# Optimization experiments

Measured on AMD Instinct MI355X. Metric: run time of the kernel, lower is better.

The kernel has to match this reference:

```python
import jax, jax.numpy as jnp
import numpy as np

B, S, D, H = 2, 2048, 1024, 16
DH = D // H  # 64


def setup_inputs() -> dict:
    key = jax.random.key(0)
    ks = jax.random.split(key, 6)
    scale = 1.0 / np.sqrt(D)
    x = jax.random.normal(ks[0], (B, S, D), dtype=jnp.float32)
    Wq = jax.random.normal(ks[1], (D, D), dtype=jnp.float32) * scale
    Wk = jax.random.normal(ks[2], (D, D), dtype=jnp.float32) * scale
    Wv = jax.random.normal(ks[3], (D, D), dtype=jnp.float32) * scale
    Wo = jax.random.normal(ks[4], (D, D), dtype=jnp.float32) * scale
    zeros = jnp.zeros((D,), dtype=jnp.float32)
    return {"x": x, "Wq": Wq, "bq": zeros, "Wk": Wk, "bk": zeros,
            "Wv": Wv, "bv": zeros, "Wo": Wo, "bo": zeros}


def reference(x, Wq, bq, Wk, bk, Wv, bv, Wo, bo):
    # x: [B, S, D]
    def split_heads(t):
        # [B, S, D] -> [B, H, S, DH]
        return t.reshape(B, S, H, DH).transpose(0, 2, 1, 3)

    q = split_heads(x @ Wq + bq)
    k = split_heads(x @ Wk + bk)
    v = split_heads(x @ Wv + bv)

    scores = jnp.einsum('bhqd,bhkd->bhqk', q, k) / jnp.sqrt(jnp.float32(DH))
    weights = jax.nn.softmax(scores, axis=-1)          # [B, H, S, S]
    o = jnp.einsum('bhqk,bhkd->bhqd', weights, v)       # [B, H, S, DH]
    o = o.transpose(0, 2, 1, 3).reshape(B, S, D)        # merge heads
    return o @ Wo + bo
```

## Files before the change

kernel.cpp:

```cpp
#include <hip/hip_runtime.h>
#include <hip/hip_bf16.h>

#define DEV __device__ __forceinline__

typedef short bf16x8 __attribute__((ext_vector_type(8)));
typedef float f32x4 __attribute__((ext_vector_type(4)));
typedef unsigned int u32;
typedef unsigned int u32x4 __attribute__((ext_vector_type(4)));

constexpr int BB = 2, SS = 2048, DD = 1024, HH = 16, DHD = 64;
constexpr int MM = BB * SS;
#define QSC 0.1803368801111f

#if __has_builtin(__builtin_amdgcn_exp2f)
#define EXP2(x) __builtin_amdgcn_exp2f(x)
#else
#define EXP2(x) exp2f(x)
#endif

DEV unsigned short f2bf(float f) {
    union { float f; unsigned int u; } v; v.f = f;
    return (unsigned short)((v.u + 0x8000u) >> 16);
}
#if __has_builtin(__builtin_amdgcn_perm)
DEV u32 pk2bf(float a, float b) {
    union { float f; u32 u; } ua, ub; ua.f = a; ub.f = b;
    return __builtin_amdgcn_perm(ub.u + 0x8000u, ua.u + 0x8000u, 0x07060302u);
}
#else
DEV u32 pk2bf(float a, float b) {
    union { float f; u32 u; } ua, ub; ua.f = a; ub.f = b;
    return ((ua.u + 0x8000u) >> 16) | ((ub.u + 0x8000u) & 0xffff0000u);
}
#endif

DEV u32 cvtpk2bf(float a, float b) {
    u32 r;
    asm("v_cvt_pk_bf16_f32 %0, %1, %2" : "=v"(r) : "v"(a), "v"(b));
    return r;
}

DEV bf16x8 ld_bf16x8(const unsigned short* p) { return *(const bf16x8*)p; }

DEV void gl16(const unsigned short* g, unsigned short* l) {
    __builtin_amdgcn_global_load_lds(
        (const __attribute__((address_space(1))) u32*)g,
        (__attribute__((address_space(3))) u32*)l, 16, 0, 0);
}

__global__ void prep(const float* __restrict__ x, unsigned short* __restrict__ xb,
                     const float* __restrict__ W0, const float* __restrict__ W1,
                     const float* __restrict__ W2, const float* __restrict__ W3,
                     unsigned short* __restrict__ WtBase) {
    __shared__ float tile[32][33];
    int blk = blockIdx.x;
    if (blk < 4096) {
        int i = blk * 256 + threadIdx.x;
        float4 v = ((const float4*)x)[i];
        uint2 o;
        o.x = pk2bf(v.x, v.y);
        o.y = pk2bf(v.z, v.w);
        ((uint2*)xb)[i] = o;
        return;
    }
    blk -= 4096;
    int wsel = blk >> 10;
    const float* W = (wsel == 0) ? W0 : (wsel == 1) ? W1 : (wsel == 2) ? W2 : W3;
    unsigned short* Wt = WtBase + (size_t)wsel * DD * DD;
    int t = blk & 1023;
    int n0 = (t & 31) * 32, k0 = (t >> 5) * 32;
    int tx = threadIdx.x & 31, ty = threadIdx.x >> 5;
    #pragma unroll
    for (int i = 0; i < 4; ++i)
        tile[ty + 8 * i][tx] = W[(size_t)(k0 + ty + 8 * i) * DD + n0 + tx];
    __syncthreads();
    #pragma unroll
    for (int i = 0; i < 4; ++i)
        Wt[(size_t)(n0 + ty + 8 * i) * DD + k0 + tx] = f2bf(tile[tx][ty + 8 * i]);
}

__global__ __launch_bounds__(256) void qkv_gemm(
    const unsigned short* __restrict__ xb,
    const unsigned short* __restrict__ WtBase,
    const float* __restrict__ bq, const float* __restrict__ bk, const float* __restrict__ bv,
    unsigned short* __restrict__ Qb, unsigned short* __restrict__ Kb, unsigned short* __restrict__ Vt)
{
    __shared__ __align__(16) unsigned short Ald[2][128 * 32];
    __shared__ __align__(16) unsigned short Bld[2][128 * 32];

    const int z = blockIdx.z;
    const unsigned short* Wt = WtBase + (size_t)z * DD * DD;
    const float* bias = (z == 0) ? bq : (z == 1) ? bk : bv;

    const int gid2 = blockIdx.x + 8 * blockIdx.y;
    const int xk = gid2 & 7, o = gid2 >> 3;
    const int xe = (xk & 1) * 4 + (o & 3);
    const int ye = (xk >> 1) * 8 + (o >> 2);
    const int m0g = ye * 128;
    const int n0g = xe * 128;

    const int wave = threadIdx.x >> 6, lane = threadIdx.x & 63;
    const int quad = lane >> 4, lcol = lane & 15;
    const int mb = (wave & 1) * 64, nb = (wave >> 1) * 64;

    f32x4 acc[4][4];
    #pragma unroll
    for (int i = 0; i < 4; ++i)
        #pragma unroll
        for (int j = 0; j < 4; ++j) acc[i][j] = (f32x4){0.f, 0.f, 0.f, 0.f};

    auto stage = [&](int ks, int bf) {
        #pragma unroll
        for (int i = 0; i < 4; ++i) {
            int j = wave * 4 + i;
            if (j < 8) {
                int bi = j * 64 + lane;
                int row = bi >> 2, p = (bi & 3) ^ ((row >> 1) & 3);
                gl16(xb + (size_t)(m0g + row) * DD + ks + p * 8, &Ald[bf][j * 512]);
            } else {
                int jj = j - 8;
                int bi = jj * 64 + lane;
                int row = bi >> 2, p = (bi & 3) ^ ((row >> 1) & 3);
                gl16(Wt + (size_t)(n0g + row) * DD + ks + p * 8, &Bld[bf][jj * 512]);
            }
        }
    };

    stage(0, 0);
    __syncthreads();

    for (int kk = 0; kk < 32; ++kk) {
        int bf = kk & 1;
        if (kk + 1 < 32) stage((kk + 1) * 32, (kk + 1) & 1);
        bf16x8 af[4], bfr[4];
        #pragma unroll
        for (int mt = 0; mt < 4; ++mt) {
            int row = mb + mt * 16 + lcol;
            af[mt] = ld_bf16x8(&Ald[bf][(row * 4 + (quad ^ ((row >> 1) & 3))) * 8]);
        }
        #pragma unroll
        for (int nt = 0; nt < 4; ++nt) {
            int row = nb + nt * 16 + lcol;
            bfr[nt] = ld_bf16x8(&Bld[bf][(row * 4 + (quad ^ ((row >> 1) & 3))) * 8]);
        }
        if (z < 2) {
            #pragma unroll
            for (int mt = 0; mt < 4; ++mt)
                #pragma unroll
                for (int nt = 0; nt < 4; ++nt)
                    acc[mt][nt] = __builtin_amdgcn_mfma_f32_16x16x32_bf16(bfr[nt], af[mt], acc[mt][nt], 0, 0, 0);
        } else {
            #pragma unroll
            for (int mt = 0; mt < 4; ++mt)
                #pragma unroll
                for (int nt = 0; nt < 4; ++nt)
                    acc[mt][nt] = __builtin_amdgcn_mfma_f32_16x16x32_bf16(af[mt], bfr[nt], acc[mt][nt], 0, 0, 0);
        }
        __syncthreads();
    }

    if (z < 2) {
        unsigned short* dst = (z == 0) ? Qb : Kb;
        const float sc = (z == 0) ? QSC : 1.0f;
        #pragma unroll
        for (int mt = 0; mt < 4; ++mt)
            #pragma unroll
            for (int nt = 0; nt < 4; ++nt) {
                int m = m0g + mb + mt * 16 + lcol;
                int nbt = n0g + nb + nt * 16 + quad * 4;
                int b = m >> 11, s = m & (SS - 1);
                int h = nbt >> 6, dh0 = nbt & 63;
                float4 bv4 = *(const float4*)&bias[nbt];
                uint2 o2;
                o2.x = pk2bf((acc[mt][nt][0] + bv4.x) * sc, (acc[mt][nt][1] + bv4.y) * sc);
                o2.y = pk2bf((acc[mt][nt][2] + bv4.z) * sc, (acc[mt][nt][3] + bv4.w) * sc);
                *(uint2*)&dst[(((size_t)b * HH + h) * SS + s) * DHD + dh0] = o2;
            }
    } else {
        #pragma unroll
        for (int mt = 0; mt < 4; ++mt)
            #pragma unroll
            for (int nt = 0; nt < 4; ++nt) {
                int n = n0g + nb + nt * 16 + lcol;
                int mbt = m0g + mb + mt * 16 + quad * 4;
                int h = n >> 6, dh = n & 63;
                int b = mbt >> 11, s0 = mbt & (SS - 1);
                float bvv = bias[n];
                uint2 o2;
                o2.x = pk2bf(acc[mt][nt][0] + bvv, acc[mt][nt][1] + bvv);
                o2.y = pk2bf(acc[mt][nt][2] + bvv, acc[mt][nt][3] + bvv);
                *(uint2*)&Vt[(((size_t)b * HH + h) * DHD + dh) * SS + s0] = o2;
            }
    }
}

__global__ __launch_bounds__(512, 4) void attn(
    const unsigned short* __restrict__ Qb,
    const unsigned short* __restrict__ Kb,
    const unsigned short* __restrict__ Vt,
    unsigned short* __restrict__ Ob)
{
    __shared__ __align__(16) unsigned short Kld[2][64 * 64];
    __shared__ __align__(16) unsigned short Vld[2][64 * 64];

    const int g = blockIdx.y * gridDim.x + blockIdx.x;
    const int bh = (g & 7) * 4 + ((g >> 3) & 3);
    const int qt = g >> 5;
    const int b = bh >> 4, h = bh & (HH - 1);
    const unsigned short* Qbh = Qb + (size_t)bh * SS * DHD;
    const unsigned short* Kbh = Kb + (size_t)bh * SS * DHD;
    const unsigned short* Vbh = Vt + (size_t)bh * DHD * SS;

    const int wave = threadIdx.x >> 6, lane = threadIdx.x & 63;
    const int quad = lane >> 4, lcol = lane & 15;
    const int rowbase = qt * 128 + wave * 16;

    bf16x8 qf0 = ld_bf16x8(Qbh + (size_t)(rowbase + lcol) * DHD + quad * 8);
    bf16x8 qf1 = ld_bf16x8(Qbh + (size_t)(rowbase + lcol) * DHD + 32 + quad * 8);

    auto krow = [&](int kf2, int j) {
        return kf2 * 32 + ((lcol >> 2) << 3) + j * 4 + (lcol & 3);
    };
    auto kswz = [](int r) { return (r & 3) | (((r >> 3) & 1) << 2); };

    auto stage = [&](int c, int bf) {
        int kb = c * 64;
        #pragma unroll
        for (int i = 0; i < 2; ++i) {
            int j = wave * 2 + i;
            if (j < 8) {
                int bi = j * 64 + lane;
                int r = bi >> 3, p = (bi & 7) ^ ((r & 3) | (((r >> 3) & 1) << 2));
                gl16(Kbh + (size_t)(kb + r) * DHD + p * 8, &Kld[bf][j * 512]);
            } else {
                int jj = j - 8;
                int bi = jj * 64 + lane;
                int dh = bi >> 3, p = (bi & 7) ^ (dh & 7);
                gl16(Vbh + (size_t)dh * SS + kb + p * 8, &Vld[bf][jj * 512]);
            }
        }
    };

    stage(0, 0);
    __syncthreads();

    float m0 = -1e30f;
    #pragma unroll
    for (int kf2 = 0; kf2 < 2; ++kf2)
        #pragma unroll
        for (int j = 0; j < 2; ++j) {
            int kr = krow(kf2, j), sw = kswz(kr);
            bf16x8 ka0 = ld_bf16x8(&Kld[0][(kr * 8 + (quad ^ sw)) * 8]);
            bf16x8 ka1 = ld_bf16x8(&Kld[0][(kr * 8 + ((quad + 4) ^ sw)) * 8]);
            f32x4 s = (f32x4){0.f, 0.f, 0.f, 0.f};
            s = __builtin_amdgcn_mfma_f32_16x16x32_bf16(ka0, qf0, s, 0, 0, 0);
            s = __builtin_amdgcn_mfma_f32_16x16x32_bf16(ka1, qf1, s, 0, 0, 0);
            #pragma unroll
            for (int r = 0; r < 4; ++r) m0 = fmaxf(m0, s[r]);
        }
    #pragma unroll
    for (int msk = 1; msk < 64; msk <<= 1) m0 = fmaxf(m0, __shfl_xor(m0, msk, 64));
    const f32x4 minit = (f32x4){-m0, -m0, -m0, -m0};

    f32x4 oacc[4];
    #pragma unroll
    for (int nt = 0; nt < 4; ++nt) oacc[nt] = (f32x4){0.f, 0.f, 0.f, 0.f};
    float ps = 0.f;

    for (int c = 0; c < 32; ++c) {
        int bf = c & 1;
        if (c + 1 < 32) stage(c + 1, (c + 1) & 1);

        bf16x8 paf[2];
        #pragma unroll
        for (int kf2 = 0; kf2 < 2; ++kf2) {
            u32 w[4];
            #pragma unroll
            for (int j = 0; j < 2; ++j) {
                int kr = krow(kf2, j), sw = kswz(kr);
                bf16x8 ka0 = ld_bf16x8(&Kld[bf][(kr * 8 + (quad ^ sw)) * 8]);
                bf16x8 ka1 = ld_bf16x8(&Kld[bf][(kr * 8 + ((quad + 4) ^ sw)) * 8]);
                f32x4 s = minit;
                s = __builtin_amdgcn_mfma_f32_16x16x32_bf16(ka0, qf0, s, 0, 0, 0);
                s = __builtin_amdgcn_mfma_f32_16x16x32_bf16(ka1, qf1, s, 0, 0, 0);
                float e0 = EXP2(s[0]), e1 = EXP2(s[1]);
                float e2 = EXP2(s[2]), e3 = EXP2(s[3]);
                ps += (e0 + e1) + (e2 + e3);
                w[j * 2]     = cvtpk2bf(e0, e1);
                w[j * 2 + 1] = cvtpk2bf(e2, e3);
            }
            union { u32x4 u; bf16x8 v; } pu;
            pu.u = (u32x4){w[0], w[1], w[2], w[3]};
            paf[kf2] = pu.v;
        }

        #pragma unroll
        for (int kf2 = 0; kf2 < 2; ++kf2) {
            #pragma unroll
            for (int nt = 0; nt < 4; ++nt) {
                int dh = nt * 16 + lcol;
                bf16x8 vb = ld_bf16x8(&Vld[bf][(dh * 8 + ((kf2 * 4 + quad) ^ (dh & 7))) * 8]);
                oacc[nt] = __builtin_amdgcn_mfma_f32_16x16x32_bf16(paf[kf2], vb, oacc[nt], 0, 0, 0);
            }
        }
        __syncthreads();
    }

    ps += __shfl_xor(ps, 16, 64);
    ps += __shfl_xor(ps, 32, 64);
    float inv = 1.0f / ps;
    #pragma unroll
    for (int r = 0; r < 4; ++r) {
        float iv = __shfl(inv, quad * 4 + r, 64);
        int srow = rowbase + quad * 4 + r;
        size_t base = (((size_t)b * SS + srow) * HH + h) * DHD;
        #pragma unroll
        for (int nt = 0; nt < 4; ++nt)
            Ob[base + nt * 16 + lcol] = f2bf(oacc[nt][r] * iv);
    }
}

__global__ __launch_bounds__(256) void out_gemm(
    const unsigned short* __restrict__ Ob,
    const unsigned short* __restrict__ Wto,
    const float* __restrict__ bo,
    float* __restrict__ out)
{
    __shared__ __align__(16) unsigned short Wld[2][128 * 64];
    __shared__ __align__(16) unsigned short Old[2][64 * 64];

    const int m0g = blockIdx.y * 64;
    const int n0g = blockIdx.x * 128;
    const int wave = threadIdx.x >> 6, lane = threadIdx.x & 63;
    const int quad = lane >> 4, lcol = lane & 15;
    const int nb = wave * 32;

    f32x4 acc[2][4];
    #pragma unroll
    for (int i = 0; i < 2; ++i)
        #pragma unroll
        for (int j = 0; j < 4; ++j) acc[i][j] = (f32x4){0.f, 0.f, 0.f, 0.f};

    auto stage = [&](int ks, int bf) {
        #pragma unroll
        for (int i = 0; i < 6; ++i) {
            int j = wave * 6 + i;
            if (j < 16) {
                int bi = j * 64 + lane;
                int r = bi >> 3, p = (bi & 7) ^ (r & 7);
                gl16(Wto + (size_t)(n0g + r) * DD + ks + p * 8, &Wld[bf][j * 512]);
            } else {
                int jj = j - 16;
                int bi = jj * 64 + lane;
                int r = bi >> 3, p = (bi & 7) ^ (r & 7);
                gl16(Ob + (size_t)(m0g + r) * DD + ks + p * 8, &Old[bf][jj * 512]);
            }
        }
    };

    stage(0, 0);
    __syncthreads();

    for (int kk = 0; kk < 16; ++kk) {
        int bf = kk & 1;
        if (kk + 1 < 16) stage((kk + 1) * 64, (kk + 1) & 1);
        #pragma unroll
        for (int kh = 0; kh < 2; ++kh) {
            bf16x8 wf[2], of[4];
            #pragma unroll
            for (int i = 0; i < 2; ++i) {
                int row = nb + i * 16 + lcol;
                wf[i] = ld_bf16x8(&Wld[bf][(row * 8 + ((kh * 4 + quad) ^ (row & 7))) * 8]);
            }
            #pragma unroll
            for (int j = 0; j < 4; ++j) {
                int row = j * 16 + lcol;
                of[j] = ld_bf16x8(&Old[bf][(row * 8 + ((kh * 4 + quad) ^ (row & 7))) * 8]);
            }
            #pragma unroll
            for (int i = 0; i < 2; ++i)
                #pragma unroll
                for (int j = 0; j < 4; ++j)
                    acc[i][j] = __builtin_amdgcn_mfma_f32_16x16x32_bf16(wf[i], of[j], acc[i][j], 0, 0, 0);
        }
        __syncthreads();
    }

    #pragma unroll
    for (int i = 0; i < 2; ++i) {
        int n4 = n0g + nb + i * 16 + quad * 4;
        float4 bv4 = *(const float4*)&bo[n4];
        #pragma unroll
        for (int j = 0; j < 4; ++j) {
            int token = m0g + j * 16 + lcol;
            float4 o;
            o.x = acc[i][j][0] + bv4.x;
            o.y = acc[i][j][1] + bv4.y;
            o.z = acc[i][j][2] + bv4.z;
            o.w = acc[i][j][3] + bv4.w;
            *(float4*)&out[(size_t)token * DD + n4] = o;
        }
    }
}

extern "C" void kernel_launch(void* const* d_in, const int* in_sizes, int n_in,
                              void* d_out, int out_size, void* d_ws, size_t ws_size,
                              hipStream_t stream)
{
    const float* x  = (const float*)d_in[0];
    const float* Wq = (const float*)d_in[1];
    const float* bq = (const float*)d_in[2];
    const float* Wk = (const float*)d_in[3];
    const float* bk = (const float*)d_in[4];
    const float* Wv = (const float*)d_in[5];
    const float* bv = (const float*)d_in[6];
    const float* Wo = (const float*)d_in[7];
    const float* bo = (const float*)d_in[8];
    float* out = (float*)d_out;

    unsigned short* ws = (unsigned short*)d_ws;
    unsigned short* Wt  = ws;
    unsigned short* Wto = Wt + 3 * (size_t)DD * DD;
    unsigned short* Qb  = Wt + 4 * (size_t)DD * DD;
    unsigned short* Kb  = Qb + (size_t)MM * DD;
    unsigned short* Vt  = Kb + (size_t)MM * DD;
    unsigned short* xb  = Vt + (size_t)MM * DD;
    unsigned short* Ob  = xb;

    prep<<<8192, 256, 0, stream>>>(x, xb, Wq, Wk, Wv, Wo, Wt);

    qkv_gemm<<<dim3(8, 32, 3), 256, 0, stream>>>(xb, Wt, bq, bk, bv, Qb, Kb, Vt);

    attn<<<dim3(16, 32), 512, 0, stream>>>(Qb, Kb, Vt, Ob);

    out_gemm<<<dim3(DD / 128, MM / 64), 256, 0, stream>>>(Ob, Wto, bo, out);
}
```

Measured before the change: 196.8 us.

## Restructure QKV GEMM into 256x256 tiles with deeper async pipeline

The QKV projection GEMM moves from 128x128 tiles with 256 threads to 256x256 tiles with 512 threads (8 waves, 128x64 per wave) on a 1D grid of 192 blocks with an XCD-aware remap. The K loop now stages 64-wide K tiles in two 32-wide halves across double buffers, with explicit vmcnt waits, barriers, sched_barriers and s_setprio around MFMA clusters so global loads overlap compute. The aim is more data reuse per LDS load and better latency hiding. The cost is more registers and LDS per block, and only 192 blocks, which may underfill the 256 CUs.

Result: slower. 229.6 us (+16.7%).

```diff
diff --git a/kernel.cpp b/kernel.cpp
--- a/kernel.cpp
+++ b/kernel.cpp
@@ -79,118 +79,163 @@
         Wt[(size_t)(n0 + ty + 8 * i) * DD + k0 + tx] = f2bf(tile[tx][ty + 8 * i]);
 }
 
-__global__ __launch_bounds__(256) void qkv_gemm(
+__global__ __launch_bounds__(512, 2) void qkv_gemm(
     const unsigned short* __restrict__ xb,
     const unsigned short* __restrict__ WtBase,
     const float* __restrict__ bq, const float* __restrict__ bk, const float* __restrict__ bv,
     unsigned short* __restrict__ Qb, unsigned short* __restrict__ Kb, unsigned short* __restrict__ Vt)
 {
-    __shared__ __align__(16) unsigned short Ald[2][128 * 32];
-    __shared__ __align__(16) unsigned short Bld[2][128 * 32];
-
-    const int z = blockIdx.z;
+    __shared__ __align__(16) unsigned short AL[2][2][256 * 32];
+    __shared__ __align__(16) unsigned short BL[2][2][256 * 32];
+
+    const int d = blockIdx.x;
+    const int w = (d & 7) * 24 + (d >> 3);
+    const int xe = w & 3, ye = (w >> 2) & 15, z = w >> 6;
+    const int m0g = ye * 256, n0g = xe * 256;
+
     const unsigned short* Wt = WtBase + (size_t)z * DD * DD;
     const float* bias = (z == 0) ? bq : (z == 1) ? bk : bv;
-
-    const int gid2 = blockIdx.x + 8 * blockIdx.y;
-    const int xk = gid2 & 7, o = gid2 >> 3;
-    const int xe = (xk & 1) * 4 + (o & 3);
-    const int ye = (xk >> 1) * 8 + (o >> 2);
-    const int m0g = ye * 128;
-    const int n0g = xe * 128;
+    const bool zlt2 = (z < 2);
 
     const int wave = threadIdx.x >> 6, lane = threadIdx.x & 63;
     const int quad = lane >> 4, lcol = lane & 15;
-    const int mb = (wave & 1) * 64, nb = (wave >> 1) * 64;
-
-    f32x4 acc[4][4];
-    #pragma unroll
-    for (int i = 0; i < 4; ++i)
+    const int wr = wave >> 2, wc = wave & 3;
+
+    f32x4 acc[8][4];
+    #pragma unroll
+    for (int i = 0; i < 8; ++i)
         #pragma unroll
         for (int j = 0; j < 4; ++j) acc[i][j] = (f32x4){0.f, 0.f, 0.f, 0.f};
 
-    auto stage = [&](int ks, int bf) {
-        #pragma unroll
-        for (int i = 0; i < 4; ++i) {
-            int j = wave * 4 + i;
-            if (j < 8) {
-                int bi = j * 64 + lane;
-                int row = bi >> 2, p = (bi & 3) ^ ((row >> 1) & 3);
-                gl16(xb + (size_t)(m0g + row) * DD + ks + p * 8, &Ald[bf][j * 512]);
-            } else {
-                int jj = j - 8;
-                int bi = jj * 64 + lane;
-                int row = bi >> 2, p = (bi & 3) ^ ((row >> 1) & 3);
-                gl16(Wt + (size_t)(n0g + row) * DD + ks + p * 8, &Bld[bf][jj * 512]);
-            }
-        }
-    };
-
-    stage(0, 0);
-    __syncthreads();
-
-    for (int kk = 0; kk < 32; ++kk) {
-        int bf = kk & 1;
-        if (kk + 1 < 32) stage((kk + 1) * 32, (kk + 1) & 1);
-        bf16x8 af[4], bfr[4];
-        #pragma unroll
-        for (int mt = 0; mt < 4; ++mt) {
-            int row = mb + mt * 16 + lcol;
-            af[mt] = ld_bf16x8(&Ald[bf][(row * 4 + (quad ^ ((row >> 1) & 3))) * 8]);
-        }
-        #pragma unroll
-        for (int nt = 0; nt < 4; ++nt) {
-            int row = nb + nt * 16 + lcol;
-            bfr[nt] = ld_bf16x8(&Bld[bf][(row * 4 + (quad ^ ((row >> 1) & 3))) * 8]);
-        }
-        if (z < 2) {
-            #pragma unroll
-            for (int mt = 0; mt < 4; ++mt)
+    auto stageA = [&](int t, int ks, int bf) {
+        #pragma unroll
+        for (int i = 0; i < 2; ++i) {
+            int j = wave * 2 + i;
+            int bi = j * 64 + lane;
+            int row = bi >> 2, p = (bi & 3) ^ ((row >> 1) & 3);
+            gl16(xb + (size_t)(m0g + row) * DD + t * 64 + ks * 32 + p * 8, &AL[bf][ks][j * 512]);
+        }
+    };
+    auto stageB = [&](int t, int ks, int bf) {
+        #pragma unroll
+        for (int i = 0; i < 2; ++i) {
+            int j = wave * 2 + i;
+            int bi = j * 64 + lane;
+            int row = bi >> 2, p = (bi & 3) ^ ((row >> 1) & 3);
+            gl16(Wt + (size_t)(n0g + row) * DD + t * 64 + ks * 32 + p * 8, &BL[bf][ks][j * 512]);
+        }
+    };
+
+    auto lda = [&](int bf, int ks, int mt) {
+        int r = wr * 128 + mt * 16 + lcol;
+        return ld_bf16x8(&AL[bf][ks][(r * 4 + (quad ^ ((r >> 1) & 3))) * 8]);
+    };
+    auto ldb = [&](int bf, int ks, int nt) {
+        int r = wc * 64 + nt * 16 + lcol;
+        return ld_bf16x8(&BL[bf][ks][(r * 4 + (quad ^ ((r >> 1) & 3))) * 8]);
+    };
+
+    auto mm16 = [&](bf16x8* a4, bf16x8* b4, int mtb) {
+        if (zlt2) {
+            #pragma unroll
+            for (int i = 0; i < 4; ++i)
                 #pragma unroll
                 for (int nt = 0; nt < 4; ++nt)
-                    acc[mt][nt] = __builtin_amdgcn_mfma_f32_16x16x32_bf16(bfr[nt], af[mt], acc[mt][nt], 0, 0, 0);
+                    acc[mtb + i][nt] = __builtin_amdgcn_mfma_f32_16x16x32_bf16(b4[nt], a4[i], acc[mtb + i][nt], 0, 0, 0);
         } else {
             #pragma unroll
-            for (int mt = 0; mt < 4; ++mt)
+            for (int i = 0; i < 4; ++i)
                 #pragma unroll
                 for (int nt = 0; nt < 4; ++nt)
-                    acc[mt][nt] = __builtin_amdgcn_mfma_f32_16x16x32_bf16(af[mt], bfr[nt], acc[mt][nt], 0, 0, 0);
-        }
-        __syncthreads();
-    }
-
-    if (z < 2) {
+                    acc[mtb + i][nt] = __builtin_amdgcn_mfma_f32_16x16x32_bf16(a4[i], b4[nt], acc[mtb + i][nt], 0, 0, 0);
+        }
+    };
+
+#define QKV_SYNC() \
+    __builtin_amdgcn_s_barrier(); \
+    asm volatile("s_waitcnt lgkmcnt(0)" ::: "memory"); \
+    __builtin_amdgcn_sched_barrier(0); \
+    __builtin_amdgcn_s_setprio(1);
+#define QKV_END() \
+    __builtin_amdgcn_s_setprio(0); \
+    __builtin_amdgcn_s_barrier(); \
+    __builtin_amdgcn_sched_barrier(0);
+
+    stageB(0, 0, 0); stageA(0, 0, 0); stageB(0, 1, 0); stageA(0, 1, 0);
+    stageB(1, 0, 1); stageA(1, 0, 1); stageB(1, 1, 1);
+    asm volatile("s_waitcnt vmcnt(6)" ::: "memory");
+    __builtin_amdgcn_s_barrier();
+    __builtin_amdgcn_sched_barrier(0);
+
+    bf16x8 a4[4], b0[4], b1[4];
+
+#define KTILE(T, BF) { \
+    const int t_ = (T); \
+     \
+    _Pragma("unroll") for (int q = 0; q < 4; ++q) b0[q] = ldb(BF, 0, q); \
+    _Pragma("unroll") for (int q = 0; q < 4; ++q) a4[q] = lda(BF, 0, q); \
+    if (t_ + 1 < 16) stageA(t_ + 1, 1, (BF) ^ 1); \
+    QKV_SYNC(); mm16(a4, b0, 0); QKV_END(); \
+     \
+    _Pragma("unroll") for (int q = 0; q < 4; ++q) a4[q] = lda(BF, 0, 4 + q); \
+    if (t_ + 2 < 16) stageB(t_ + 2, 0, BF); \
+    QKV_SYNC(); mm16(a4, b0, 4); QKV_END(); \
+     \
+    _Pragma("unroll") for (int q = 0; q < 4; ++q) b1[q] = ldb(BF, 1, q); \
+    _Pragma("unroll") for (int q = 0; q < 4; ++q) a4[q] = lda(BF, 1, q); \
+    if (t_ + 2 < 16) stageA(t_ + 2, 0, BF); \
+    QKV_SYNC(); mm16(a4, b1, 0); QKV_END(); \
+     \
+    _Pragma("unroll") for (int q = 0; q < 4; ++q) a4[q] = lda(BF, 1, 4 + q); \
+    if (t_ + 2 < 16) stageB(t_ + 2, 1, BF); \
+    if (t_ <= 13) { asm volatile("s_waitcnt vmcnt(6)" ::: "memory"); } \
+    else if (t_ == 14) { asm volatile("s_waitcnt vmcnt(0)" ::: "memory"); } \
+    QKV_SYNC(); mm16(a4, b1, 4); QKV_END(); \
+}
+
+    #pragma unroll 1
+    for (int tt = 0; tt < 16; tt += 2) {
+        KTILE(tt, 0);
+        KTILE(tt + 1, 1);
+    }
+#undef KTILE
+#undef QKV_SYNC
+#undef QKV_END
+
+    if (zlt2) {
         unsigned short* dst = (z == 0) ? Qb : Kb;
         const float sc = (z == 0) ? QSC : 1.0f;
         #pragma unroll
-        for (int mt = 0; mt < 4; ++mt)
+        for (int mt = 0; mt < 8; ++mt) {
+            int m = m0g + wr * 128 + mt * 16 + lcol;
+            int b_ = m >> 11, s = m & (SS - 1);
             #pragma unroll
             for (int nt = 0; nt < 4; ++nt) {
-                int m = m0g + mb + mt * 16 + lcol;
-                int nbt = n0g + nb + nt * 16 + quad * 4;
-                int b = m >> 11, s = m & (SS - 1);
+                int nbt = n0g + wc * 64 + nt * 16 + quad * 4;
                 int h = nbt >> 6, dh0 = nbt & 63;
                 float4 bv4 = *(const float4*)&bias[nbt];
                 uint2 o2;
                 o2.x = pk2bf((acc[mt][nt][0] + bv4.x) * sc, (acc[mt][nt][1] + bv4.y) * sc);
                 o2.y = pk2bf((acc[mt][nt][2] + bv4.z) * sc, (acc[mt][nt][3] + bv4.w) * sc);
-                *(uint2*)&dst[(((size_t)b * HH + h) * SS + s) * DHD + dh0] = o2;
-            }
+                *(uint2*)&dst[(((size_t)b_ * HH + h) * SS + s) * DHD + dh0] = o2;
+            }
+        }
     } else {
         #pragma unroll
-        for (int mt = 0; mt < 4; ++mt)
+        for (int mt = 0; mt < 8; ++mt) {
+            int mbt = m0g + wr * 128 + mt * 16 + quad * 4;
+            int b_ = mbt >> 11, s0 = mbt & (SS - 1);
             #pragma unroll
             for (int nt = 0; nt < 4; ++nt) {
-                int n = n0g + nb + nt * 16 + lcol;
-                int mbt = m0g + mb + mt * 16 + quad * 4;
+                int n = n0g + wc * 64 + nt * 16 + lcol;
                 int h = n >> 6, dh = n & 63;
-                int b = mbt >> 11, s0 = mbt & (SS - 1);
                 float bvv = bias[n];
                 uint2 o2;
                 o2.x = pk2bf(acc[mt][nt][0] + bvv, acc[mt][nt][1] + bvv);
                 o2.y = pk2bf(acc[mt][nt][2] + bvv, acc[mt][nt][3] + bvv);
-                *(uint2*)&Vt[(((size_t)b * HH + h) * DHD + dh) * SS + s0] = o2;
-            }
+                *(uint2*)&Vt[(((size_t)b_ * HH + h) * DHD + dh) * SS + s0] = o2;
+            }
+        }
     }
 }
 
@@ -429,7 +474,7 @@
 
     prep<<<8192, 256, 0, stream>>>(x, xb, Wq, Wk, Wv, Wo, Wt);
 
-    qkv_gemm<<<dim3(8, 32, 3), 256, 0, stream>>>(xb, Wt, bq, bk, bv, Qb, Kb, Vt);
+    qkv_gemm<<<dim3(192), 512, 0, stream>>>(xb, Wt, bq, bk, bv, Qb, Kb, Vt);
 
     attn<<<dim3(16, 32), 512, 0, stream>>>(Qb, Kb, Vt, Ob);
 
```
